# Kernel optimization log

Hardware: AMD Instinct MI355X
Metric: run time of the kernel (lower is better)

Reference implementation:

```python
import jax, jax.numpy as jnp
import numpy as np

MARGIN = 0.3
N, D = 8192, 1024
NUM_IDS = 751

def setup_inputs() -> dict:
    key = jax.random.key(0)
    k1, k2 = jax.random.split(key)
    inputs = jax.random.normal(k1, (N, D), dtype=jnp.float32)
    targets = jax.random.randint(k2, (N,), 0, NUM_IDS, dtype=jnp.int64)
    return {"inputs": inputs, "targets": targets}

def reference(inputs, targets):
    # sim[i,j] = <x_i, x_j>
    sim = jnp.matmul(inputs, inputs.T)  # [N, N]
    same = targets[:, None] == targets[None, :]  # [N, N] bool
    # positives: same label AND sim < 1 -> contribute (1 - sim)
    pos_mask = same & (sim < 1.0)
    pos_loss = jnp.sum(jnp.where(pos_mask, 1.0 - sim, 0.0), axis=1)  # [N]
    # negatives: different label AND sim > margin -> contribute sim
    neg_mask = (~same) & (sim > MARGIN)
    neg_loss = jnp.sum(jnp.where(neg_mask, sim, 0.0), axis=1)  # [N]
    n = inputs.shape[0]
    return jnp.sum(pos_loss + neg_loss) / n
```

## Files before the change

### kernel.cpp

```cpp
#include <hip/hip_runtime.h>
#include <stdint.h>

typedef float f32x4 __attribute__((ext_vector_type(4)));

#define NROWS 8192
#define DIM   1024
#define BK    128
#define NKT   (DIM / BK)
#define MARGIN 0.3f

#define GLOAD_LDS16(gp, lp)                                                    \
  __builtin_amdgcn_global_load_lds(                                            \
      (const __attribute__((address_space(1))) void*)(gp),                     \
      (__attribute__((address_space(3))) void*)(lp), 16, 0, 0)

__global__ __launch_bounds__(256) void cvt_f32_fp8(const float* __restrict__ in,
                                                   uint8_t* __restrict__ out,
                                                   float* __restrict__ loss) {
  if (blockIdx.x == 0 && threadIdx.x == 0) loss[0] = 0.0f;
  size_t i = ((size_t)blockIdx.x * 256 + threadIdx.x) * 16;
  float4 v0 = *(const float4*)(in + i);
  float4 v1 = *(const float4*)(in + i + 4);
  float4 v2 = *(const float4*)(in + i + 8);
  float4 v3 = *(const float4*)(in + i + 12);
  int w0 = 0, w1 = 0, w2 = 0, w3 = 0;
  w0 = __builtin_amdgcn_cvt_pk_fp8_f32(v0.x, v0.y, w0, false);
  w0 = __builtin_amdgcn_cvt_pk_fp8_f32(v0.z, v0.w, w0, true);
  w1 = __builtin_amdgcn_cvt_pk_fp8_f32(v1.x, v1.y, w1, false);
  w1 = __builtin_amdgcn_cvt_pk_fp8_f32(v1.z, v1.w, w1, true);
  w2 = __builtin_amdgcn_cvt_pk_fp8_f32(v2.x, v2.y, w2, false);
  w2 = __builtin_amdgcn_cvt_pk_fp8_f32(v2.z, v2.w, w2, true);
  w3 = __builtin_amdgcn_cvt_pk_fp8_f32(v3.x, v3.y, w3, false);
  w3 = __builtin_amdgcn_cvt_pk_fp8_f32(v3.z, v3.w, w3, true);
  uint4 p; p.x = (unsigned)w0; p.y = (unsigned)w1; p.z = (unsigned)w2; p.w = (unsigned)w3;
  *(uint4*)(out + i) = p;
}

__global__ __launch_bounds__(256, 3) void gram_loss(const uint8_t* __restrict__ A8,
                                                    const int* __restrict__ targets,
                                                    float* __restrict__ out) {
  __shared__ uint8_t As[128 * 128];
  __shared__ uint8_t Bs[128 * 128];
  __shared__ int tRow[128];
  __shared__ int tCol[128];
  __shared__ float wsum[4];

  int t = blockIdx.x;
  int bi = (int)(0.5f * (129.0f - __builtin_sqrtf(129.0f * 129.0f - 8.0f * (float)t)));
  if (bi < 0) bi = 0;
  if (bi > 63) bi = 63;
  while (bi < 63 && ((bi + 1) * (129 - (bi + 1))) / 2 <= t) ++bi;
  while (bi > 0 && (bi * (129 - bi)) / 2 > t) --bi;
  int bj = bi + (t - (bi * (129 - bi)) / 2);

  const int iBase = bi * 128;
  const int jBase = bj * 128;

  const int tid  = threadIdx.x;
  const int wave = tid >> 6;
  const int lane = tid & 63;

  if (tid < 128) tRow[tid] = targets[iBase + tid];
  else           tCol[tid - 128] = targets[jBase + tid - 128];

  const int lrow = lane >> 3;
  const int cg   = (lane & 7) ^ lrow;
  const uint8_t* gA = A8 + (size_t)(iBase + wave * 32 + lrow) * DIM + cg * 16;
  const uint8_t* gB = A8 + (size_t)(jBase + wave * 32 + lrow) * DIM + cg * 16;
  uint8_t* lA = &As[wave * 32 * 128];
  uint8_t* lB = &Bs[wave * 32 * 128];

  const int m0 = (wave >> 1) * 64;
  const int n0 = (wave & 1) * 64;
  const int fr = lane & 15;
  const int h  = lane >> 4;
  const int r7 = fr & 7;
  const int hHi = h >> 1;
  const int hLo = (h & 1) * 8;

  f32x4 acc[4][4] = {};

  for (int kt = 0; kt < NKT; ++kt) {
    __syncthreads();
    const int kOff = kt * BK;
#pragma unroll
    for (int l = 0; l < 4; ++l)
      GLOAD_LDS16(gA + (size_t)(l * 8) * DIM + kOff, lA + l * 8 * 128);
#pragma unroll
    for (int l = 0; l < 4; ++l)
      GLOAD_LDS16(gB + (size_t)(l * 8) * DIM + kOff, lB + l * 8 * 128);
    __syncthreads();

#pragma unroll
    for (int ks = 0; ks < 4; ++ks) {
      const int colOff = (((ks * 2 + hHi) ^ r7) * 16) + hLo;
      long af[4], bf[4];
#pragma unroll
      for (int mi = 0; mi < 4; ++mi)
        af[mi] = *(const long*)&As[(m0 + mi * 16 + fr) * 128 + colOff];
#pragma unroll
      for (int ni = 0; ni < 4; ++ni)
        bf[ni] = *(const long*)&Bs[(n0 + ni * 16 + fr) * 128 + colOff];
#pragma unroll
      for (int mi = 0; mi < 4; ++mi)
#pragma unroll
        for (int ni = 0; ni < 4; ++ni)
          acc[mi][ni] = __builtin_amdgcn_mfma_f32_16x16x32_fp8_fp8(
              af[mi], bf[ni], acc[mi][ni], 0, 0, 0);
    }
  }

  const int col = lane & 15;
  const int rquad = (lane >> 4) * 4;
  float lsum = 0.0f;
#pragma unroll
  for (int ni = 0; ni < 4; ++ni) {
    const int tj = tCol[n0 + ni * 16 + col];
#pragma unroll
    for (int mi = 0; mi < 4; ++mi) {
#pragma unroll
      for (int r = 0; r < 4; ++r) {
        float s = acc[mi][ni][r];
        int ti = tRow[m0 + mi * 16 + rquad + r];
        lsum += (ti == tj) ? (s < 1.0f ? 1.0f - s : 0.0f)
                           : (s > MARGIN ? s : 0.0f);
      }
    }
  }
  if (bi != bj) lsum *= 2.0f;

#pragma unroll
  for (int off = 32; off > 0; off >>= 1) lsum += __shfl_down(lsum, off, 64);
  if (lane == 0) wsum[wave] = lsum;
  __syncthreads();
  if (tid == 0)
    atomicAdd(out, (wsum[0] + wsum[1] + wsum[2] + wsum[3]) * (1.0f / (float)NROWS));
}

extern "C" void kernel_launch(void* const* d_in, const int* in_sizes, int n_in,
                              void* d_out, int out_size, void* d_ws, size_t ws_size,
                              hipStream_t stream) {
  const float* x = (const float*)d_in[0];
  const int* targets = (const int*)d_in[1];
  float* out = (float*)d_out;
  uint8_t* x8 = (uint8_t*)d_ws;

  cvt_f32_fp8<<<2048, 256, 0, stream>>>(x, x8, out);
  gram_loss<<<2080, 256, 0, stream>>>(x8, targets, out);
}
```

Before: 136.4 us.

## Prefetch next K tile into registers to overlap global loads with MFMA

Replaces direct global-to-LDS loads with register staging. The next K tile is loaded into registers while the current tile's MFMAs run, then written to swizzled LDS at the top of the next iteration. The aim is to hide global memory latency behind compute. The cost is extra VGPRs for the staging buffers, which may reduce occupancy under launch_bounds(256,3), plus an explicit LDS write step.

```diff
diff --git a/kernel.cpp b/kernel.cpp
--- a/kernel.cpp
+++ b/kernel.cpp
@@ -8,11 +8,6 @@
 #define BK    128
 #define NKT   (DIM / BK)
 #define MARGIN 0.3f
-
-#define GLOAD_LDS16(gp, lp)                                                    \
-  __builtin_amdgcn_global_load_lds(                                            \
-      (const __attribute__((address_space(1))) void*)(gp),                     \
-      (__attribute__((address_space(3))) void*)(lp), 16, 0, 0)
 
 __global__ __launch_bounds__(256) void cvt_f32_fp8(const float* __restrict__ in,
                                                    uint8_t* __restrict__ out,
@@ -64,11 +59,11 @@
   else           tCol[tid - 128] = targets[jBase + tid - 128];
 
   const int lrow = lane >> 3;
-  const int cg   = (lane & 7) ^ lrow;
-  const uint8_t* gA = A8 + (size_t)(iBase + wave * 32 + lrow) * DIM + cg * 16;
-  const uint8_t* gB = A8 + (size_t)(jBase + wave * 32 + lrow) * DIM + cg * 16;
-  uint8_t* lA = &As[wave * 32 * 128];
-  uint8_t* lB = &Bs[wave * 32 * 128];
+  const int cgl  = lane & 7;
+  const uint8_t* gA = A8 + (size_t)(iBase + wave * 32 + lrow) * DIM + cgl * 16;
+  const uint8_t* gB = A8 + (size_t)(jBase + wave * 32 + lrow) * DIM + cgl * 16;
+  uint8_t* lA = &As[(wave * 32 + lrow) * 128 + ((cgl ^ lrow) * 16)];
+  uint8_t* lB = &Bs[(wave * 32 + lrow) * 128 + ((cgl ^ lrow) * 16)];
 
   const int m0 = (wave >> 1) * 64;
   const int n0 = (wave & 1) * 64;
@@ -80,16 +75,30 @@
 
   f32x4 acc[4][4] = {};
 
+  uint4 ga[4], gb[4];
+#pragma unroll
+  for (int l = 0; l < 4; ++l) {
+    ga[l] = *(const uint4*)(gA + (size_t)(l * 8) * DIM);
+    gb[l] = *(const uint4*)(gB + (size_t)(l * 8) * DIM);
+  }
+
   for (int kt = 0; kt < NKT; ++kt) {
     __syncthreads();
-    const int kOff = kt * BK;
 #pragma unroll
-    for (int l = 0; l < 4; ++l)
-      GLOAD_LDS16(gA + (size_t)(l * 8) * DIM + kOff, lA + l * 8 * 128);
+    for (int l = 0; l < 4; ++l) {
+      *(uint4*)(lA + l * 8 * 128) = ga[l];
+      *(uint4*)(lB + l * 8 * 128) = gb[l];
+    }
+    __syncthreads();
+
+    if (kt + 1 < NKT) {
+      const int kOff = (kt + 1) * BK;
 #pragma unroll
-    for (int l = 0; l < 4; ++l)
-      GLOAD_LDS16(gB + (size_t)(l * 8) * DIM + kOff, lB + l * 8 * 128);
-    __syncthreads();
+      for (int l = 0; l < 4; ++l) {
+        ga[l] = *(const uint4*)(gA + (size_t)(l * 8) * DIM + kOff);
+        gb[l] = *(const uint4*)(gB + (size_t)(l * 8) * DIM + kOff);
+      }
+    }
 
 #pragma unroll
     for (int ks = 0; ks < 4; ++ks) {
```

Result: slower. 285.5 us (+109.3%).

## Double K tile to 256 with 16-way swizzle and per-wave A/B load split

Applied to the files above, without the earlier changes.

The k-tile is doubled from 128 to 256 bytes, so each tile now needs 4 k-iterations and fewer barrier pairs. The LDS layout changes to a 16-way XOR swizzle over the 256-byte rows. Loads are split so two waves fill A and two fill B, each loading 64 rows. The fp8 convert kernel now handles 4 floats per thread with a 4x larger grid. LDS use rises to 64KB per block and the occupancy hint of 3 is dropped, which may lower occupancy.

```diff
diff --git a/kernel.cpp b/kernel.cpp
--- a/kernel.cpp
+++ b/kernel.cpp
@@ -5,7 +5,7 @@
 
 #define NROWS 8192
 #define DIM   1024
-#define BK    128
+#define BK    256
 #define NKT   (DIM / BK)
 #define MARGIN 0.3f
 
@@ -18,29 +18,19 @@
                                                    uint8_t* __restrict__ out,
                                                    float* __restrict__ loss) {
   if (blockIdx.x == 0 && threadIdx.x == 0) loss[0] = 0.0f;
-  size_t i = ((size_t)blockIdx.x * 256 + threadIdx.x) * 16;
-  float4 v0 = *(const float4*)(in + i);
-  float4 v1 = *(const float4*)(in + i + 4);
-  float4 v2 = *(const float4*)(in + i + 8);
-  float4 v3 = *(const float4*)(in + i + 12);
-  int w0 = 0, w1 = 0, w2 = 0, w3 = 0;
-  w0 = __builtin_amdgcn_cvt_pk_fp8_f32(v0.x, v0.y, w0, false);
-  w0 = __builtin_amdgcn_cvt_pk_fp8_f32(v0.z, v0.w, w0, true);
-  w1 = __builtin_amdgcn_cvt_pk_fp8_f32(v1.x, v1.y, w1, false);
-  w1 = __builtin_amdgcn_cvt_pk_fp8_f32(v1.z, v1.w, w1, true);
-  w2 = __builtin_amdgcn_cvt_pk_fp8_f32(v2.x, v2.y, w2, false);
-  w2 = __builtin_amdgcn_cvt_pk_fp8_f32(v2.z, v2.w, w2, true);
-  w3 = __builtin_amdgcn_cvt_pk_fp8_f32(v3.x, v3.y, w3, false);
-  w3 = __builtin_amdgcn_cvt_pk_fp8_f32(v3.z, v3.w, w3, true);
-  uint4 p; p.x = (unsigned)w0; p.y = (unsigned)w1; p.z = (unsigned)w2; p.w = (unsigned)w3;
-  *(uint4*)(out + i) = p;
+  size_t i = ((size_t)blockIdx.x * 256 + threadIdx.x) * 4;
+  float4 v = *(const float4*)(in + i);
+  int w = 0;
+  w = __builtin_amdgcn_cvt_pk_fp8_f32(v.x, v.y, w, false);
+  w = __builtin_amdgcn_cvt_pk_fp8_f32(v.z, v.w, w, true);
+  *(unsigned*)(out + i) = (unsigned)w;
 }
 
-__global__ __launch_bounds__(256, 3) void gram_loss(const uint8_t* __restrict__ A8,
-                                                    const int* __restrict__ targets,
-                                                    float* __restrict__ out) {
-  __shared__ uint8_t As[128 * 128];
-  __shared__ uint8_t Bs[128 * 128];
+__global__ __launch_bounds__(256) void gram_loss(const uint8_t* __restrict__ A8,
+                                                 const int* __restrict__ targets,
+                                                 float* __restrict__ out) {
+  __shared__ uint8_t As[128 * 256];
+  __shared__ uint8_t Bs[128 * 256];
   __shared__ int tRow[128];
   __shared__ int tCol[128];
   __shared__ float wsum[4];
@@ -63,18 +53,17 @@
   if (tid < 128) tRow[tid] = targets[iBase + tid];
   else           tCol[tid - 128] = targets[jBase + tid - 128];
 
-  const int lrow = lane >> 3;
-  const int cg   = (lane & 7) ^ lrow;
-  const uint8_t* gA = A8 + (size_t)(iBase + wave * 32 + lrow) * DIM + cg * 16;
-  const uint8_t* gB = A8 + (size_t)(jBase + wave * 32 + lrow) * DIM + cg * 16;
-  uint8_t* lA = &As[wave * 32 * 128];
-  uint8_t* lB = &Bs[wave * 32 * 128];
+  const int half = wave & 1;
+  const int isB  = wave >> 1;
+  const int lrow = lane >> 4;
+  const int cs   = lane & 15;
+  const uint8_t* gBase = A8 + (size_t)((isB ? jBase : iBase) + half * 64) * DIM;
+  uint8_t* lT = (isB ? Bs : As) + half * 64 * 256;
 
   const int m0 = (wave >> 1) * 64;
   const int n0 = (wave & 1) * 64;
   const int fr = lane & 15;
   const int h  = lane >> 4;
-  const int r7 = fr & 7;
   const int hHi = h >> 1;
   const int hLo = (h & 1) * 8;
 
@@ -84,23 +73,23 @@
     __syncthreads();
     const int kOff = kt * BK;
 #pragma unroll
-    for (int l = 0; l < 4; ++l)
-      GLOAD_LDS16(gA + (size_t)(l * 8) * DIM + kOff, lA + l * 8 * 128);
-#pragma unroll
-    for (int l = 0; l < 4; ++l)
-      GLOAD_LDS16(gB + (size_t)(l * 8) * DIM + kOff, lB + l * 8 * 128);
+    for (int l = 0; l < 16; ++l) {
+      const int r = l * 4 + lrow;
+      const int scg = cs ^ (r & 15);
+      GLOAD_LDS16(gBase + (size_t)r * DIM + kOff + scg * 16, lT + l * 1024);
+    }
     __syncthreads();
 
 #pragma unroll
-    for (int ks = 0; ks < 4; ++ks) {
-      const int colOff = (((ks * 2 + hHi) ^ r7) * 16) + hLo;
+    for (int ks = 0; ks < 8; ++ks) {
+      const int colOff = (((ks * 2 + hHi) ^ fr) * 16) + hLo;
       long af[4], bf[4];
 #pragma unroll
       for (int mi = 0; mi < 4; ++mi)
-        af[mi] = *(const long*)&As[(m0 + mi * 16 + fr) * 128 + colOff];
+        af[mi] = *(const long*)&As[(m0 + mi * 16 + fr) * 256 + colOff];
 #pragma unroll
       for (int ni = 0; ni < 4; ++ni)
-        bf[ni] = *(const long*)&Bs[(n0 + ni * 16 + fr) * 128 + colOff];
+        bf[ni] = *(const long*)&Bs[(n0 + ni * 16 + fr) * 256 + colOff];
 #pragma unroll
       for (int mi = 0; mi < 4; ++mi)
 #pragma unroll
@@ -145,6 +134,6 @@
   float* out = (float*)d_out;
   uint8_t* x8 = (uint8_t*)d_ws;
 
-  cvt_f32_fp8<<<2048, 256, 0, stream>>>(x, x8, out);
+  cvt_f32_fp8<<<8192, 256, 0, stream>>>(x, x8, out);
   gram_loss<<<2080, 256, 0, stream>>>(x8, targets, out);
 }
```

Result: slower. 151.0 us (+10.7%).
